# Performance work log

Hardware: AMD Instinct MI355X
Metric: run time of the kernel (lower is better)

## Reference

```python
import jax, jax.numpy as jnp
import numpy as np


def ste_round(x):
    # straight-through rounding (identity gradient), as used in brevitas fake-quant
    return x + jax.lax.stop_gradient(jnp.round(x) - x)


def quant_weight(w, bits):
    # symmetric per-tensor int quantization: scale = max|w| / (2^(b-1)-1)
    qmax = 2.0 ** (bits - 1) - 1.0
    s = jnp.max(jnp.abs(w)) / qmax
    return jnp.clip(ste_round(w / s), -qmax, qmax) * s


def quant_relu(x, scale, bits):
    # unsigned act quant (QuantReLU): clip to [0, scale], round to 2^b-1 levels
    n = 2.0 ** bits - 1.0
    step = scale / n
    return ste_round(jnp.clip(x, 0.0, scale) / step) * step


def conv2d(x, w, b, pad):
    # NCHW 'same' conv, stride 1
    y = jax.lax.conv_general_dilated(
        x, w, window_strides=(1, 1),
        padding=[(pad, pad), (pad, pad)],
        dimension_numbers=('NCHW', 'OIHW', 'NCHW'))
    return y + b[None, :, None, None]


def setup_inputs() -> dict:
    key = jax.random.key(0)
    ks = jax.random.split(key, 8)
    B, H, W = 8, 512, 512
    x = jax.random.uniform(ks[0], (B, 1, H, W), dtype=jnp.float32)
    # xavier-ish init scales: gain / sqrt(fan_in + fan_out per kernel elem)
    w1 = jax.random.normal(ks[1], (64, 1, 9, 9), dtype=jnp.float32) * 0.12
    b1 = jax.random.normal(ks[2], (64,), dtype=jnp.float32) * 0.01
    w2 = jax.random.normal(ks[3], (32, 64, 5, 5), dtype=jnp.float32) * 0.03
    b2 = jax.random.normal(ks[4], (32,), dtype=jnp.float32) * 0.01
    w3 = jax.random.normal(ks[5], (1, 32, 5, 5), dtype=jnp.float32) * 0.05
    b3 = jax.random.normal(ks[6], (1,), dtype=jnp.float32) * 0.01
    # activation quant scales (learned params in brevitas; fixed here)
    s1 = jnp.ones((1,), dtype=jnp.float32) * 4.0
    s2 = jnp.ones((1,), dtype=jnp.float32) * 4.0
    s3 = jnp.ones((1,), dtype=jnp.float32) * 2.0
    return {"x": x, "w1": w1, "b1": b1, "w2": w2, "b2": b2,
            "w3": w3, "b3": b3, "s1": s1, "s2": s2, "s3": s3}


def reference(x, w1, b1, w2, b2, w3, b3, s1, s2, s3):
    NBK, NBA, NLACT = 8, 8, 8
    # conv1: 1->64, k=9, pad=4, int8 weights; quant-ReLU (nba bits)
    h = conv2d(x, quant_weight(w1, NBK), b1, pad=4)
    h = quant_relu(h, s1[0], NBA)
    # conv2: 64->32, k=5, pad=2
    h = conv2d(h, quant_weight(w2, NBK), b2, pad=2)
    h = quant_relu(h, s2[0], NBA)
    # conv3: 32->1, k=5, pad=2, last-layer weight bits = nlact = 8
    h = conv2d(h, quant_weight(w3, NLACT), b3, pad=2)
    h = quant_relu(h, s3[0], NLACT)
    return h
```

## Files before the change

kernel.cpp:

```cpp
#include <hip/hip_runtime.h>
#include <cmath>

#define HH 512
#define WW 512
#define BB 8
#define WP (WW + 4)
#define HP (HH + 4)

#define PROWS 520
#define PCOLS 528
#define PT ((size_t)BB * PROWS * PCOLS)

typedef int v4i __attribute__((ext_vector_type(4)));
typedef float v4f __attribute__((ext_vector_type(4)));
typedef _Float16 v8h __attribute__((ext_vector_type(8)));

#if defined(__has_builtin)
#if __has_builtin(__builtin_amdgcn_sdot4)
#define DOT4(a, b, c) __builtin_amdgcn_sdot4((a), (b), (c), false)
#endif
#endif
#ifndef DOT4
static __device__ __forceinline__ int dot4_fb(int a, int b, int c) {
  c += ((a << 24) >> 24) * ((b << 24) >> 24);
  c += ((a << 16) >> 24) * ((b << 16) >> 24);
  c += ((a << 8) >> 24) * ((b << 8) >> 24);
  c += (a >> 24) * (b >> 24);
  return c;
}
#define DOT4(a, b, c) dot4_fb((a), (b), (c))
#endif

static constexpr size_t SCALES_OFF = 0;
static constexpr size_t CORRF_OFF  = 64;
static constexpr size_t FS3_OFF    = 512;
static constexpr size_t QW1_OFF    = 1024;
static constexpr size_t W1FRAG_OFF = 24576;
static constexpr size_t W2S_OFF    = 65536;
static constexpr size_t W3P_OFF    = 131072;
static constexpr size_t H1_OFF     = (size_t)1 << 20;
static constexpr size_t H1_SZ      = (size_t)BB * HP * WP * 64;
static constexpr size_t H2_OFF     = H1_OFF + H1_SZ;
static constexpr size_t H2_SZ      = (size_t)BB * HP * WP * 32;
static constexpr size_t WS_NEED    = H2_OFF + H2_SZ;

__global__ void quant_weights_k(const float* __restrict__ w1,
                                const float* __restrict__ w2,
                                const float* __restrict__ w3,
                                float* __restrict__ scales,
                                float* __restrict__ qw1,
                                signed char* __restrict__ w2s,
                                signed char* __restrict__ w3p) {
  const int t = blockIdx.x;
  const float* src = (t == 0) ? w1 : (t == 1) ? w2 : w3;
  const int n = (t == 0) ? 64 * 81 : (t == 1) ? 32 * 64 * 25 : 32 * 25;
  __shared__ float red[256];
  float m = 0.0f;
  for (int i = threadIdx.x; i < n; i += 256) m = fmaxf(m, fabsf(src[i]));
  red[threadIdx.x] = m;
  __syncthreads();
  for (int s = 128; s > 0; s >>= 1) {
    if ((int)threadIdx.x < s) red[threadIdx.x] = fmaxf(red[threadIdx.x], red[threadIdx.x + s]);
    __syncthreads();
  }
  const float scale = red[0] / 127.0f;
  if (threadIdx.x == 0) scales[t] = scale;
  for (int i = threadIdx.x; i < n; i += 256) {
    float q = rintf(src[i] / scale);
    q = fminf(fmaxf(q, -127.0f), 127.0f);
    if (t == 0) {
      qw1[i] = q;
    } else if (t == 1) {
      const int oc = i / 1600;
      const int r = i - oc * 1600;
      const int ic = r / 25, tap = r - ic * 25;
      w2s[(((tap * 4 + (ic >> 4)) * 32) + oc) * 16 + (ic & 15)] = (signed char)(int)q;
    } else {
      const int ic = i / 25, tap = i - ic * 25;
      w3p[tap * 32 + ic] = (signed char)(int)q;
    }
  }
}

__global__ void prep_k(const signed char* __restrict__ w2s,
                       const signed char* __restrict__ w3p,
                       const float* __restrict__ qw1,
                       int* __restrict__ corrf, int* __restrict__ fs3,
                       unsigned short* __restrict__ w1frag) {
  const int tid = threadIdx.x;
  if (tid < 32) {
    int s = 0;
    for (int tap = 0; tap < 25; ++tap)
      for (int kb = 0; kb < 4; ++kb)
        for (int j = 0; j < 16; ++j)
          s += (int)w2s[((tap * 4 + kb) * 32 + tid) * 16 + j];
    corrf[tid] = s;
  } else if (tid == 32) {
    int s = 0;
    for (int i = 0; i < 800; ++i) s += (int)w3p[i];
    fs3[0] = s;
  }
  for (int i = tid; i < 18432; i += 256) {
    const int e = i & 7, lidx = (i >> 3) & 63, nn = (i >> 9) & 3, j = i >> 11;
    const int t = j * 32 + (lidx >> 4) * 8 + e;
    const int term = (t >= 144) ? 1 : 0;
    const int rem = t - term * 144;
    const int ky = rem >> 4, kx = rem & 15;
    const int oc = nn * 16 + (lidx & 15);
    float v = 0.0f;
    if (kx < 9) v = qw1[oc * 81 + ky * 9 + kx];
    if (term) v *= (1.0f / 4096.0f);
    const _Float16 hv = (_Float16)v;
    w1frag[i] = __builtin_bit_cast(unsigned short, hv);
  }
}

__global__ __launch_bounds__(256) void prep_x_k(const float* __restrict__ x,
                                                unsigned short* __restrict__ planes) {
  const size_t i = (size_t)blockIdx.x * 256 + threadIdx.x;
  if (i >= PT) return;
  const int col = (int)(i % PCOLS);
  const size_t t = i / PCOLS;
  const int row = (int)(t % PROWS);
  const int b = (int)(t / PROWS);
  const float* xb = x + (size_t)b * HH * WW;
  const int xr = row - 4;
  float v0 = 0.0f, v1 = 0.0f;
  if (xr >= 0 && xr < HH) {
    const int c0 = col - 4, c1 = col - 3;
    if (c0 >= 0 && c0 < WW) v0 = xb[(size_t)xr * WW + c0];
    if (c1 >= 0 && c1 < WW) v1 = xb[(size_t)xr * WW + c1];
  }
  const _Float16 h0 = (_Float16)v0;
  const _Float16 l0 = (_Float16)((v0 - (float)h0) * 4096.0f);
  const _Float16 h1 = (_Float16)v1;
  const _Float16 l1 = (_Float16)((v1 - (float)h1) * 4096.0f);
  planes[i]          = __builtin_bit_cast(unsigned short, h0);
  planes[PT + i]     = __builtin_bit_cast(unsigned short, l0);
  planes[2 * PT + i] = __builtin_bit_cast(unsigned short, h1);
  planes[3 * PT + i] = __builtin_bit_cast(unsigned short, l1);
}

__global__ void fill_k(unsigned char* __restrict__ h1p, unsigned char* __restrict__ h2p) {
  const int idx = blockIdx.x * 256 + threadIdx.x;
  const uint4 v = make_uint4(0x80808080u, 0x80808080u, 0x80808080u, 0x80808080u);
  if (idx < 66048) {
    const int q = idx & 3; const int u = idx >> 2;
    const int pxi = u % WP; const int rr = u / WP;
    const int bb = rr >> 2, sel = rr & 3;
    const int row = (sel < 2) ? sel : 512 + sel;
    *(uint4*)(h1p + (((size_t)bb * HP + row) * WP + pxi) * 64 + q * 16) = v;
  } else if (idx < 131584) {
    const int e = idx - 66048; const int q = e & 3; int u = e >> 2;
    const int c = u & 3; u >>= 2;
    const int row = 2 + (u & 511); const int bb = u >> 9;
    const int col = (c < 2) ? c : 512 + c;
    *(uint4*)(h1p + (((size_t)bb * HP + row) * WP + col) * 64 + q * 16) = v;
  } else if (idx < 164608) {
    const int e = idx - 131584; const int q = e & 1; const int u = e >> 1;
    const int pxi = u % WP; const int rr = u / WP;
    const int bb = rr >> 2, sel = rr & 3;
    const int row = (sel < 2) ? sel : 512 + sel;
    *(uint4*)(h2p + (((size_t)bb * HP + row) * WP + pxi) * 32 + q * 16) = v;
  } else {
    const int e = idx - 164608; const int q = e & 1; int u = e >> 1;
    const int c = u & 3; u >>= 2;
    const int row = 2 + (u & 511); const int bb = u >> 9;
    const int col = (c < 2) ? c : 512 + c;
    *(uint4*)(h2p + (((size_t)bb * HP + row) * WP + col) * 32 + q * 16) = v;
  }
}

__global__ __launch_bounds__(512) void conv1_k(
    const unsigned short* __restrict__ planes,
    const unsigned short* __restrict__ w1frag,
    const float* __restrict__ b1,
    const float* __restrict__ scales,
    const float* __restrict__ s1,
    unsigned char* __restrict__ h1p) {
  __shared__ alignas(16) unsigned short wf[18432];
  for (int i = threadIdx.x; i < 2304; i += 512)
    ((int4*)wf)[i] = ((const int4*)w1frag)[i];
  __syncthreads();

  const int y = blockIdx.x & (HH - 1);
  const int b = blockIdx.x >> 9;
  const int l = threadIdx.x & 63;
  const int wv = threadIdx.x >> 6;
  const int pxw = wv * 64;
  const int r = l & 15, kb = l >> 4;

  const unsigned short* pb = planes + (size_t)(r & 1) * (2 * PT)
                           + ((size_t)b * PROWS + y) * PCOLS + (pxw + (r & ~1));
  int offs[9];
  #pragma unroll
  for (int j = 0; j < 9; ++j) {
    const int t0 = j * 32 + kb * 8;
    const int term = (t0 >= 144) ? 1 : 0;
    const int rem = t0 - term * 144;
    offs[j] = term * (int)PT + (rem >> 4) * PCOLS + (rem & 8);
  }

  v4f acc[4][4];
  #pragma unroll
  for (int p = 0; p < 4; ++p)
    #pragma unroll
    for (int o = 0; o < 4; ++o) acc[p][o] = (v4f){0.f, 0.f, 0.f, 0.f};

  #pragma unroll
  for (int j = 0; j < 9; ++j) {
    v8h av[4];
    #pragma unroll
    for (int p = 0; p < 4; ++p) {
      const void* ap = __builtin_assume_aligned((const void*)(pb + offs[j] + p * 16), 4);
      uint4 tv;
      __builtin_memcpy(&tv, ap, 16);
      av[p] = __builtin_bit_cast(v8h, tv);
    }
    #pragma unroll
    for (int o = 0; o < 4; ++o) {
      const v8h bw = *(const v8h*)(wf + ((size_t)(j * 4 + o) * 64 + l) * 8);
      #pragma unroll
      for (int p = 0; p < 4; ++p)
        acc[p][o] = __builtin_amdgcn_mfma_f32_16x16x32_f16(bw, av[p], acc[p][o], 0, 0, 0);
    }
  }

  const float ws1 = scales[0];
  const float sc = s1[0], step = sc / 255.0f;
  unsigned int* ob = (unsigned int*)(h1p
      + (((size_t)b * HP + y + 2) * WP + 2 + pxw + r) * 64 + kb * 4);
  #pragma unroll
  for (int o = 0; o < 4; ++o) {
    const v4f bv = *(const v4f*)(b1 + o * 16 + kb * 4);
    #pragma unroll
    for (int p = 0; p < 4; ++p) {
      unsigned int dw = 0;
      #pragma unroll
      for (int reg = 0; reg < 4; ++reg) {
        const float h = acc[p][o][reg] * ws1 + bv[reg];
        const float c = fminf(fmaxf(h, 0.0f), sc);
        int qi = (int)rintf(c / step);
        qi = qi < 0 ? 0 : (qi > 255 ? 255 : qi);
        dw |= (unsigned int)(qi ^ 0x80) << (8 * reg);
      }
      ob[p * 256 + o * 4] = dw;
    }
  }
}

__global__ __launch_bounds__(256) void conv2_k(
    const unsigned char* __restrict__ h1p,
    const int4* __restrict__ w2s,
    const int* __restrict__ corrf,
    const float* __restrict__ b2,
    const float* __restrict__ scales,
    const float* __restrict__ s1, const float* __restrict__ s2,
    unsigned char* __restrict__ h2p) {
  __shared__ alignas(16) signed char wlds[51200];
  __shared__ alignas(16) int clds[32];
  {
    int4* dst = (int4*)wlds;
    for (int i = threadIdx.x; i < 3200; i += 256) dst[i] = w2s[i];
    if (threadIdx.x < 32) clds[threadIdx.x] = corrf[threadIdx.x];
  }
  __syncthreads();

  const int l = threadIdx.x & 63;
  const int wv = threadIdx.x >> 6;
  const int r = l & 15, kb = l >> 4;
  const int y = blockIdx.y * 4;
  const int b = blockIdx.z;
  const int xw = blockIdx.x * 64 + wv * 16;

  v4i acc[4][2];
  #pragma unroll
  for (int t = 0; t < 4; ++t)
    #pragma unroll
    for (int n = 0; n < 2; ++n) acc[t][n] = (v4i){0, 0, 0, 0};

  const size_t rstride = (size_t)WP * 64;
  const unsigned char* abase = h1p + (((size_t)b * HP + y) * WP + xw + r) * 64 + kb * 16;

  v4i a_cur[8], a_nxt[8];
  #pragma unroll
  for (int j = 0; j < 8; ++j) a_cur[j] = *(const v4i*)(abase + j * rstride);

  #pragma unroll
  for (int kx = 0; kx < 5; ++kx) {
    if (kx < 4) {
      #pragma unroll
      for (int j = 0; j < 8; ++j)
        a_nxt[j] = *(const v4i*)(abase + (kx + 1) * 64 + j * rstride);
    }
    const signed char* bcol = wlds + kx * 2048 + kb * 512 + r * 16;
    #pragma unroll
    for (int ky = 0; ky < 5; ++ky) {
      const v4i bf0 = *(const v4i*)(bcol + ky * 10240);
      const v4i bf1 = *(const v4i*)(bcol + ky * 10240 + 256);
      #pragma unroll
      for (int t = 0; t < 4; ++t) {
        acc[t][0] = __builtin_amdgcn_mfma_i32_16x16x64_i8(bf0, a_cur[ky + t], acc[t][0], 0, 0, 0);
        acc[t][1] = __builtin_amdgcn_mfma_i32_16x16x64_i8(bf1, a_cur[ky + t], acc[t][1], 0, 0, 0);
      }
    }
    if (kx < 4) {
      #pragma unroll
      for (int j = 0; j < 8; ++j) a_cur[j] = a_nxt[j];
    }
  }

  const float step1 = s1[0] / 255.0f;
  const float sc2 = s2[0], step2 = sc2 / 255.0f;
  const float asc = step1 * scales[1];
  #pragma unroll
  for (int n = 0; n < 2; ++n) {
    const v4f bv = *(const v4f*)(b2 + n * 16 + kb * 4);
    const v4i cv = *(const v4i*)(clds + n * 16 + kb * 4);
    #pragma unroll
    for (int t = 0; t < 4; ++t) {
      unsigned int* ob = (unsigned int*)(h2p
          + (((size_t)b * HP + y + t + 2) * WP + xw + 2 + r) * 32 + n * 16 + kb * 4);
      unsigned int dw = 0;
      #pragma unroll
      for (int reg = 0; reg < 4; ++reg) {
        const float v = (float)(acc[t][n][reg] + cv[reg] * 128) * asc + bv[reg];
        const float c = fminf(fmaxf(v, 0.0f), sc2);
        int qi = (int)rintf(c / step2);
        qi = qi < 0 ? 0 : (qi > 255 ? 255 : qi);
        dw |= (unsigned int)(qi ^ 0x80) << (8 * reg);
      }
      *ob = dw;
    }
  }
}

__global__ __launch_bounds__(256) void conv3_k(
    const unsigned char* __restrict__ h2p,
    const signed char* __restrict__ w3p,
    const int* __restrict__ fs3,
    const float* __restrict__ b3,
    const float* __restrict__ scales,
    const float* __restrict__ s2, const float* __restrict__ s3,
    float* __restrict__ out) {
  const int p  = blockIdx.x * 256 + threadIdx.x;
  const int px = p & (WW - 1);
  const int py = (p >> 9) & (HH - 1);
  const int bz = p >> 18;

  const int* wq = (const int*)w3p;
  const unsigned char* base = h2p + (((size_t)bz * HP + py) * WP + px) * 32;

  int acc = 0;
  #pragma unroll
  for (int ky = 0; ky < 5; ++ky) {
    const v4i* rp = (const v4i*)(base + (size_t)ky * WP * 32);
    v4i c[10];
    #pragma unroll
    for (int g = 0; g < 10; ++g) c[g] = rp[g];
    const int* wrow = wq + ky * 40;
    #pragma unroll
    for (int kx = 0; kx < 5; ++kx) {
      #pragma unroll
      for (int g = 0; g < 8; ++g) {
        const int idx = kx * 8 + g;
        acc = DOT4(c[idx >> 2][idx & 3], wrow[idx], acc);
      }
    }
  }

  const int tot = acc + fs3[0] * 128;
  const float step2 = s2[0] / 255.0f;
  const float sc3 = s3[0], step3 = sc3 / 255.0f;
  const float y = (float)tot * (step2 * scales[2]) + b3[0];
  const float c = fminf(fmaxf(y, 0.0f), sc3);
  float q = rintf(c / step3);
  q = fminf(fmaxf(q, 0.0f), 255.0f);
  out[p] = q * step3;
}

extern "C" void kernel_launch(void* const* d_in, const int* in_sizes, int n_in,
                              void* d_out, int out_size, void* d_ws, size_t ws_size,
                              hipStream_t stream) {
  const float* x  = (const float*)d_in[0];
  const float* w1 = (const float*)d_in[1];
  const float* b1 = (const float*)d_in[2];
  const float* w2 = (const float*)d_in[3];
  const float* b2 = (const float*)d_in[4];
  const float* w3 = (const float*)d_in[5];
  const float* b3 = (const float*)d_in[6];
  const float* s1 = (const float*)d_in[7];
  const float* s2 = (const float*)d_in[8];
  const float* s3 = (const float*)d_in[9];

  if (ws_size < WS_NEED) return;

  char* ws = (char*)d_ws;
  float*          scales  = (float*)(ws + SCALES_OFF);
  int*            corrf   = (int*)(ws + CORRF_OFF);
  int*            fs3     = (int*)(ws + FS3_OFF);
  float*          qw1     = (float*)(ws + QW1_OFF);
  unsigned short* w1frag  = (unsigned short*)(ws + W1FRAG_OFF);
  signed char*    w2s     = (signed char*)(ws + W2S_OFF);
  signed char*    w3p     = (signed char*)(ws + W3P_OFF);
  unsigned char*  h1p     = (unsigned char*)(ws + H1_OFF);
  unsigned char*  h2p     = (unsigned char*)(ws + H2_OFF);
  unsigned short* planes  = (unsigned short*)(ws + H2_OFF);

  quant_weights_k<<<3, 256, 0, stream>>>(w1, w2, w3, scales, qw1, w2s, w3p);
  prep_k<<<1, 256, 0, stream>>>(w2s, w3p, qw1, corrf, fs3, w1frag);
  prep_x_k<<<(int)(PT / 256), 256, 0, stream>>>(x, planes);

  conv1_k<<<BB * HH, 512, 0, stream>>>(planes, w1frag, b1, scales, s1, h1p);
  fill_k<<<771, 256, 0, stream>>>(h1p, h2p);

  dim3 g2(8, 128, BB);
  conv2_k<<<g2, 256, 0, stream>>>(h1p, (const int4*)w2s, corrf, b2, scales, s1, s2, h2p);

  const int npix = BB * HH * WW;
  conv3_k<<<npix / 256, 256, 0, stream>>>(h2p, w3p, fs3, b3, scales, s2, s3, (float*)d_out);
}
```

Baseline: 473.5 us.

## Read conv2 weights from global/L2 instead of staging in LDS; parallelize prep sums

conv2_k no longer copies the 51 KB int8 weight tensor into shared memory with a barrier per block. MFMA weight fragments are now loaded directly from global memory, relying on L1/L2 caching since every block reads the same weights. This removes the per-block staging cost and the large LDS allocation that limited occupancy, but puts global-load latency on the inner loop. prep_k also computes its weight row sums in parallel with dot4 and shuffle reductions instead of serial loops.

```diff
diff --git a/kernel.cpp b/kernel.cpp
--- a/kernel.cpp
+++ b/kernel.cpp
@@ -88,16 +88,36 @@
                        int* __restrict__ corrf, int* __restrict__ fs3,
                        unsigned short* __restrict__ w1frag) {
   const int tid = threadIdx.x;
+  __shared__ int red3[32];
+  {
+    const int oc = tid >> 3, part = tid & 7;
+    const unsigned int* wd = (const unsigned int*)w2s;
+    int s = 0;
+    for (int chunk = part; chunk < 100; chunk += 8) {
+      const int tap = chunk >> 2, kb = chunk & 3;
+      const int base = tap * 512 + kb * 128 + oc * 4;
+      #pragma unroll
+      for (int j = 0; j < 4; ++j) s = DOT4((int)wd[base + j], 0x01010101, s);
+    }
+    s += __shfl_xor(s, 1);
+    s += __shfl_xor(s, 2);
+    s += __shfl_xor(s, 4);
+    if (part == 0) corrf[oc] = s;
+  }
   if (tid < 32) {
     int s = 0;
-    for (int tap = 0; tap < 25; ++tap)
-      for (int kb = 0; kb < 4; ++kb)
-        for (int j = 0; j < 16; ++j)
-          s += (int)w2s[((tap * 4 + kb) * 32 + tid) * 16 + j];
-    corrf[tid] = s;
-  } else if (tid == 32) {
+    if (tid < 25) {
+      const unsigned int* wd = (const unsigned int*)w3p;
+      #pragma unroll
+      for (int j = 0; j < 8; ++j) s = DOT4((int)wd[tid * 8 + j], 0x01010101, s);
+    }
+    red3[tid] = s;
+  }
+  __syncthreads();
+  if (tid == 0) {
     int s = 0;
-    for (int i = 0; i < 800; ++i) s += (int)w3p[i];
+    #pragma unroll
+    for (int j = 0; j < 32; ++j) s += red3[j];
     fs3[0] = s;
   }
   for (int i = tid; i < 18432; i += 256) {
@@ -251,21 +271,12 @@
 
 __global__ __launch_bounds__(256) void conv2_k(
     const unsigned char* __restrict__ h1p,
-    const int4* __restrict__ w2s,
+    const signed char* __restrict__ w2g,
     const int* __restrict__ corrf,
     const float* __restrict__ b2,
     const float* __restrict__ scales,
     const float* __restrict__ s1, const float* __restrict__ s2,
     unsigned char* __restrict__ h2p) {
-  __shared__ alignas(16) signed char wlds[51200];
-  __shared__ alignas(16) int clds[32];
-  {
-    int4* dst = (int4*)wlds;
-    for (int i = threadIdx.x; i < 3200; i += 256) dst[i] = w2s[i];
-    if (threadIdx.x < 32) clds[threadIdx.x] = corrf[threadIdx.x];
-  }
-  __syncthreads();
-
   const int l = threadIdx.x & 63;
   const int wv = threadIdx.x >> 6;
   const int r = l & 15, kb = l >> 4;
@@ -281,6 +292,7 @@
 
   const size_t rstride = (size_t)WP * 64;
   const unsigned char* abase = h1p + (((size_t)b * HP + y) * WP + xw + r) * 64 + kb * 16;
+  const signed char* wl = w2g + kb * 512 + r * 16;
 
   v4i a_cur[8], a_nxt[8];
   #pragma unroll
@@ -293,11 +305,11 @@
       for (int j = 0; j < 8; ++j)
         a_nxt[j] = *(const v4i*)(abase + (kx + 1) * 64 + j * rstride);
     }
-    const signed char* bcol = wlds + kx * 2048 + kb * 512 + r * 16;
     #pragma unroll
     for (int ky = 0; ky < 5; ++ky) {
-      const v4i bf0 = *(const v4i*)(bcol + ky * 10240);
-      const v4i bf1 = *(const v4i*)(bcol + ky * 10240 + 256);
+      const signed char* wt = wl + (ky * 5 + kx) * 2048;
+      const v4i bf0 = *(const v4i*)(wt);
+      const v4i bf1 = *(const v4i*)(wt + 256);
       #pragma unroll
       for (int t = 0; t < 4; ++t) {
         acc[t][0] = __builtin_amdgcn_mfma_i32_16x16x64_i8(bf0, a_cur[ky + t], acc[t][0], 0, 0, 0);
@@ -316,7 +328,7 @@
   #pragma unroll
   for (int n = 0; n < 2; ++n) {
     const v4f bv = *(const v4f*)(b2 + n * 16 + kb * 4);
-    const v4i cv = *(const v4i*)(clds + n * 16 + kb * 4);
+    const v4i cv = *(const v4i*)(corrf + n * 16 + kb * 4);
     #pragma unroll
     for (int t = 0; t < 4; ++t) {
       unsigned int* ob = (unsigned int*)(h2p
@@ -415,7 +427,7 @@
   fill_k<<<771, 256, 0, stream>>>(h1p, h2p);
 
   dim3 g2(8, 128, BB);
-  conv2_k<<<g2, 256, 0, stream>>>(h1p, (const int4*)w2s, corrf, b2, scales, s1, s2, h2p);
+  conv2_k<<<g2, 256, 0, stream>>>(h1p, w2s, corrf, b2, scales, s1, s2, h2p);
 
   const int npix = BB * HH * WW;
   conv3_k<<<npix / 256, 256, 0, stream>>>(h2p, w3p, fs3, b3, scales, s2, s3, (float*)d_out);
```

Result: slower. 487.0 us (+2.8%).
